# Performance work log

Measured on AMD Instinct MI355X. Metric: run time of the kernel, lower is better.

## Reference

```python
import jax, jax.numpy as jnp
import numpy as np

ALPHA = 0.2
EMB_DIM = 128
IMG = 48


def setup_inputs() -> dict:
    key = jax.random.key(0)
    k1, k2, k3, k4 = jax.random.split(key, 4)
    B = 8192
    batch_anchor = jax.random.normal(k1, (B, 1, IMG, IMG), dtype=jnp.float32)
    batch_pos = jax.random.normal(k2, (B, 1, IMG, IMG), dtype=jnp.float32)
    batch_neg = jax.random.normal(k3, (B, 1, IMG, IMG), dtype=jnp.float32)
    W = jax.random.normal(k4, (IMG * IMG, EMB_DIM), dtype=jnp.float32) * (1.0 / np.sqrt(IMG * IMG))
    b = jnp.zeros((EMB_DIM,), dtype=jnp.float32)
    return {"batch_anchor": batch_anchor, "batch_pos": batch_pos, "batch_neg": batch_neg, "W": W, "b": b}


def _encode(x, W, b):
    # x: [B, 1, 48, 48] -> flatten -> linear -> [B, emb]
    B = x.shape[0]
    return x.reshape(B, -1) @ W + b


def reference(batch_anchor, batch_pos, batch_neg, W, b):
    emb_a = _encode(batch_anchor, W, b)
    emb_p = _encode(batch_pos, W, b)
    emb_n = _encode(batch_neg, W, b)
    d_ap = jnp.sum((emb_a - emb_p) ** 2, axis=-1)  # squared distance, [B]
    d_an = jnp.sum((emb_a - emb_n) ** 2, axis=-1)
    loss = jax.nn.relu(d_ap - d_an + ALPHA)
    return jnp.mean(loss)
```

## Files before the change

### kernel.cpp

```cpp
#include <hip/hip_runtime.h>
#include <hip/hip_bf16.h>


#define KDIM  2304
#define EMBD  128
#define BATCH 8192
#define KCH   72
#define NT    8
#define NW    8
#define CPW   9
#define ALPHA 0.2f

typedef __attribute__((ext_vector_type(8))) short short8;
typedef __attribute__((ext_vector_type(4))) float f32x4;

__device__ __forceinline__ unsigned short f2bf(float f) {
    unsigned u = __builtin_bit_cast(unsigned, f);
    u += 0x7FFFu + ((u >> 16) & 1u);
    return (unsigned short)(u >> 16);
}

__global__ void pack_w_kernel(const float* __restrict__ W,
                              unsigned short* __restrict__ Wp) {
    int tid = blockIdx.x * blockDim.x + threadIdx.x;
    int n = tid & 127;
    int k = tid >> 7;
    int c = k >> 5;
    int q = (k >> 3) & 3;
    int j = k & 7;
    int t = n >> 4;
    int l = q * 16 + (n & 15);
    Wp[(size_t)(((c * 8 + t) * 64) + l) * 8 + j] = f2bf(W[tid]);
}

__global__ __launch_bounds__(512, 4) void triplet_kernel(
    const float* __restrict__ A, const float* __restrict__ P,
    const float* __restrict__ Ng, const unsigned short* __restrict__ Wp,
    float* __restrict__ out)
{
    __shared__ float lds[4][2][NT][64][4];

    const int lane = threadIdx.x & 63;
    const int wave = threadIdx.x >> 6;
    const int m    = lane & 15;
    const int q    = lane >> 4;
    const int c0   = wave * CPW;

    const size_t rowoff = (size_t)(blockIdx.x * 16 + m) * KDIM + q * 8;
    const f32x4* pa = (const f32x4*)(A  + rowoff) + (size_t)c0 * 8;
    const f32x4* pp = (const f32x4*)(P  + rowoff) + (size_t)c0 * 8;
    const f32x4* pn = (const f32x4*)(Ng + rowoff) + (size_t)c0 * 8;
    const short8* wp = (const short8*)Wp + lane + (size_t)c0 * NT * 64;

    f32x4 aU[NT], aV[NT];
#pragma unroll
    for (int t = 0; t < NT; ++t) {
        aU[t] = (f32x4){0.f, 0.f, 0.f, 0.f};
        aV[t] = (f32x4){0.f, 0.f, 0.f, 0.f};
    }

#pragma unroll 3
    for (int c = 0; c < CPW; ++c) {
        f32x4 a0 = pa[c * 8], a1 = pa[c * 8 + 1];
        f32x4 p0 = pp[c * 8], p1 = pp[c * 8 + 1];
        f32x4 n0 = pn[c * 8], n1 = pn[c * 8 + 1];
        f32x4 u0 = a0 - p0, u1 = a1 - p1;
        f32x4 v0 = a0 - n0, v1 = a1 - n1;
        short8 uf, vf;
#pragma unroll
        for (int i = 0; i < 4; ++i) {
            uf[i]     = (short)f2bf(u0[i]);
            uf[i + 4] = (short)f2bf(u1[i]);
            vf[i]     = (short)f2bf(v0[i]);
            vf[i + 4] = (short)f2bf(v1[i]);
        }
        const short8* wc = wp + (size_t)c * NT * 64;
#pragma unroll
        for (int t = 0; t < NT; ++t) {
            short8 bf = wc[t * 64];
            aU[t] = __builtin_amdgcn_mfma_f32_16x16x32_bf16(uf, bf, aU[t], 0, 0, 0);
            aV[t] = __builtin_amdgcn_mfma_f32_16x16x32_bf16(vf, bf, aV[t], 0, 0, 0);
        }
    }

#define STORE_FRAGS(r)                                              \
    do {                                                            \
        _Pragma("unroll")                                           \
        for (int t = 0; t < NT; ++t) {                              \
            *(f32x4*)&lds[r][0][t][lane][0] = aU[t];                \
            *(f32x4*)&lds[r][1][t][lane][0] = aV[t];                \
        }                                                           \
    } while (0)
#define ADD_FRAGS(r)                                                \
    do {                                                            \
        _Pragma("unroll")                                           \
        for (int t = 0; t < NT; ++t) {                              \
            aU[t] += *(const f32x4*)&lds[r][0][t][lane][0];         \
            aV[t] += *(const f32x4*)&lds[r][1][t][lane][0];         \
        }                                                           \
    } while (0)

    if (wave >= 4) STORE_FRAGS(wave - 4);
    __syncthreads();
    if (wave < 4) ADD_FRAGS(wave);
    __syncthreads();
    if (wave == 2 || wave == 3) STORE_FRAGS(wave - 2);
    __syncthreads();
    if (wave < 2) ADD_FRAGS(wave);
    __syncthreads();
    if (wave == 1) STORE_FRAGS(0);
    __syncthreads();

    if (wave == 0) {
        ADD_FRAGS(0);
        float du[4] = {0.f, 0.f, 0.f, 0.f};
        float dv[4] = {0.f, 0.f, 0.f, 0.f};
#pragma unroll
        for (int t = 0; t < NT; ++t) {
#pragma unroll
            for (int r = 0; r < 4; ++r) {
                du[r] += aU[t][r] * aU[t][r];
                dv[r] += aV[t][r] * aV[t][r];
            }
        }
#pragma unroll
        for (int msk = 1; msk < 16; msk <<= 1) {
#pragma unroll
            for (int r = 0; r < 4; ++r) {
                du[r] += __shfl_xor(du[r], msk, 64);
                dv[r] += __shfl_xor(dv[r], msk, 64);
            }
        }
        float s = 0.f;
#pragma unroll
        for (int r = 0; r < 4; ++r) {
            float l = du[r] - dv[r] + ALPHA;
            s += l > 0.f ? l : 0.f;
        }
        s += __shfl_xor(s, 16, 64);
        s += __shfl_xor(s, 32, 64);
        if (lane == 0) atomicAdd(out, s * (1.0f / BATCH));
    }
}

extern "C" void kernel_launch(void* const* d_in, const int* in_sizes, int n_in,
                              void* d_out, int out_size, void* d_ws, size_t ws_size,
                              hipStream_t stream) {
    const float* A  = (const float*)d_in[0];
    const float* P  = (const float*)d_in[1];
    const float* Ng = (const float*)d_in[2];
    const float* W  = (const float*)d_in[3];
    unsigned short* Wp = (unsigned short*)d_ws;

    hipMemsetAsync(d_out, 0, sizeof(float), stream);

    pack_w_kernel<<<(KDIM * EMBD) / 256, 256, 0, stream>>>(W, Wp);
    triplet_kernel<<<BATCH / 16, 512, 0, stream>>>(A, P, Ng, Wp, (float*)d_out);
}
```

Baseline: 243.5 us.

## Double-buffer activation loads via global_load_lds with per-wave prefetch

Activation tiles for anchor, positive and negative are now staged into per-wave double-buffered LDS through direct global-to-LDS loads, so the next chunk is prefetched while the current chunk is computed. The bf16 conversion uses a packed hardware convert instruction, and W fragments are loaded at the top of each iteration. LDS use grows to 96 KB per block and launch bounds drop to 2 blocks per SIMD, which lowers occupancy. Hand-written waitcnt and inline asm add a risk of fragile ordering.

New measurement: 236.4 us. -2.9%, faster.

```diff
diff --git a/kernel.cpp b/kernel.cpp
--- a/kernel.cpp
+++ b/kernel.cpp
@@ -1,11 +1,9 @@
 #include <hip/hip_runtime.h>
-#include <hip/hip_bf16.h>
 
 
 #define KDIM  2304
 #define EMBD  128
 #define BATCH 8192
-#define KCH   72
 #define NT    8
 #define NW    8
 #define CPW   9
@@ -13,6 +11,10 @@
 
 typedef __attribute__((ext_vector_type(8))) short short8;
 typedef __attribute__((ext_vector_type(4))) float f32x4;
+typedef __attribute__((ext_vector_type(4))) unsigned int u32x4;
+
+#define AS1 __attribute__((address_space(1)))
+#define AS3 __attribute__((address_space(3)))
 
 __device__ __forceinline__ unsigned short f2bf(float f) {
     unsigned u = __builtin_bit_cast(unsigned, f);
@@ -33,23 +35,52 @@
     Wp[(size_t)(((c * 8 + t) * 64) + l) * 8 + j] = f2bf(W[tid]);
 }
 
-__global__ __launch_bounds__(512, 4) void triplet_kernel(
+__device__ __forceinline__ unsigned cvtpk(float lo, float hi) {
+    unsigned r;
+    asm("v_cvt_pk_bf16_f32 %0, %1, %2" : "=v"(r) : "v"(lo), "v"(hi));
+    return r;
+}
+
+__device__ __forceinline__ void gll16(const float* g, char* l) {
+    __builtin_amdgcn_global_load_lds((AS1 void*)(void*)g, (AS3 void*)l, 16, 0, 0);
+}
+
+__device__ __forceinline__ void lds_read6(const char* p, f32x4& a0, f32x4& a1,
+                                          f32x4& p0, f32x4& p1,
+                                          f32x4& n0, f32x4& n1) {
+    const AS3 char* lp = (const AS3 char*)p;
+    asm volatile(
+        "ds_read_b128 %0, %6 offset:0\n\t"
+        "ds_read_b128 %1, %6 offset:1024\n\t"
+        "ds_read_b128 %2, %6 offset:2048\n\t"
+        "ds_read_b128 %3, %6 offset:3072\n\t"
+        "ds_read_b128 %4, %6 offset:4096\n\t"
+        "ds_read_b128 %5, %6 offset:5120\n\t"
+        "s_waitcnt lgkmcnt(0)"
+        : "=&v"(a0), "=&v"(a1), "=&v"(p0), "=&v"(p1), "=&v"(n0), "=&v"(n1)
+        : "v"(lp)
+        : "memory");
+}
+
+__global__ __launch_bounds__(512, 2) void triplet_kernel(
     const float* __restrict__ A, const float* __restrict__ P,
     const float* __restrict__ Ng, const unsigned short* __restrict__ Wp,
     float* __restrict__ out)
 {
-    __shared__ float lds[4][2][NT][64][4];
+    __shared__ __align__(16) char smem[NW * 12288];
 
     const int lane = threadIdx.x & 63;
     const int wave = threadIdx.x >> 6;
-    const int m    = lane & 15;
-    const int q    = lane >> 4;
     const int c0   = wave * CPW;
 
-    const size_t rowoff = (size_t)(blockIdx.x * 16 + m) * KDIM + q * 8;
-    const f32x4* pa = (const f32x4*)(A  + rowoff) + (size_t)c0 * 8;
-    const f32x4* pp = (const f32x4*)(P  + rowoff) + (size_t)c0 * 8;
-    const f32x4* pn = (const f32x4*)(Ng + rowoff) + (size_t)c0 * 8;
+    const size_t goff = (size_t)(blockIdx.x * 16 + (lane & 15)) * KDIM
+                      + (size_t)(lane >> 4) * 8 + (size_t)c0 * 32;
+    const float* gA = A  + goff;
+    const float* gP = P  + goff;
+    const float* gN = Ng + goff;
+
+    char* wb = smem + wave * 12288;
+
     const short8* wp = (const short8*)Wp + lane + (size_t)c0 * NT * 64;
 
     f32x4 aU[NT], aV[NT];
@@ -59,29 +90,61 @@
         aV[t] = (f32x4){0.f, 0.f, 0.f, 0.f};
     }
 
-#pragma unroll 3
+#define STAGE(cc, bufoff)                                   \
+    do {                                                    \
+        const float* _a = gA + (cc) * 32;                   \
+        const float* _p = gP + (cc) * 32;                   \
+        const float* _n = gN + (cc) * 32;                   \
+        char* _b = wb + (bufoff);                           \
+        gll16(_a,     _b);                                  \
+        gll16(_a + 4, _b + 1024);                           \
+        gll16(_p,     _b + 2048);                           \
+        gll16(_p + 4, _b + 3072);                           \
+        gll16(_n,     _b + 4096);                           \
+        gll16(_n + 4, _b + 5120);                           \
+    } while (0)
+
+    STAGE(0, 0);
+
+    const char* rp0 = wb + lane * 16;
+    const char* rp1 = wb + 6144 + lane * 16;
+
+#pragma unroll
     for (int c = 0; c < CPW; ++c) {
-        f32x4 a0 = pa[c * 8], a1 = pa[c * 8 + 1];
-        f32x4 p0 = pp[c * 8], p1 = pp[c * 8 + 1];
-        f32x4 n0 = pn[c * 8], n1 = pn[c * 8 + 1];
-        f32x4 u0 = a0 - p0, u1 = a1 - p1;
-        f32x4 v0 = a0 - n0, v1 = a1 - n1;
-        short8 uf, vf;
-#pragma unroll
-        for (int i = 0; i < 4; ++i) {
-            uf[i]     = (short)f2bf(u0[i]);
-            uf[i + 4] = (short)f2bf(u1[i]);
-            vf[i]     = (short)f2bf(v0[i]);
-            vf[i + 4] = (short)f2bf(v1[i]);
-        }
-        const short8* wc = wp + (size_t)c * NT * 64;
+        short8 wf[NT];
+#pragma unroll
+        for (int t = 0; t < NT; ++t) wf[t] = wp[c * 512 + t * 64];
+
+        if (c + 1 < CPW) {
+            STAGE(c + 1, ((c + 1) & 1) * 6144);
+            asm volatile("s_waitcnt vmcnt(6)" ::: "memory");
+        } else {
+            asm volatile("s_waitcnt vmcnt(0)" ::: "memory");
+        }
+
+        f32x4 xa0, xa1, xp0, xp1, xn0, xn1;
+        lds_read6((c & 1) ? rp1 : rp0, xa0, xa1, xp0, xp1, xn0, xn1);
+
+        f32x4 ul = xa0 - xp0, uh = xa1 - xp1;
+        f32x4 vl = xa0 - xn0, vh = xa1 - xn1;
+        u32x4 uw, vw;
+        uw[0] = cvtpk(ul[0], ul[1]); uw[1] = cvtpk(ul[2], ul[3]);
+        uw[2] = cvtpk(uh[0], uh[1]); uw[3] = cvtpk(uh[2], uh[3]);
+        vw[0] = cvtpk(vl[0], vl[1]); vw[1] = cvtpk(vl[2], vl[3]);
+        vw[2] = cvtpk(vh[0], vh[1]); vw[3] = cvtpk(vh[2], vh[3]);
+        short8 uf = __builtin_bit_cast(short8, uw);
+        short8 vf = __builtin_bit_cast(short8, vw);
+
 #pragma unroll
         for (int t = 0; t < NT; ++t) {
-            short8 bf = wc[t * 64];
-            aU[t] = __builtin_amdgcn_mfma_f32_16x16x32_bf16(uf, bf, aU[t], 0, 0, 0);
-            aV[t] = __builtin_amdgcn_mfma_f32_16x16x32_bf16(vf, bf, aV[t], 0, 0, 0);
+            aU[t] = __builtin_amdgcn_mfma_f32_16x16x32_bf16(uf, wf[t], aU[t], 0, 0, 0);
+            aV[t] = __builtin_amdgcn_mfma_f32_16x16x32_bf16(vf, wf[t], aV[t], 0, 0, 0);
         }
     }
+
+    __syncthreads();
+
+    float (*lds)[2][NT][64][4] = (float(*)[2][NT][64][4])(void*)smem;
 
 #define STORE_FRAGS(r)                                              \
     do {                                                            \
```
